# Kernel optimization log

Measured on AMD Instinct MI355X. Metric: run time of the kernel, lower is better.

Reference implementation:

```python
import jax, jax.numpy as jnp
import numpy as np

B, C, H, W = 1, 512, 64, 64
HEADS, DIM_HEAD = 8, 64
GROUPS = 32
EPS = 1e-5
SCALE = DIM_HEAD ** -0.5


def setup_inputs() -> dict:
    key = jax.random.key(0)
    ks = jax.random.split(key, 8)
    inner = HEADS * DIM_HEAD  # 512
    s = 0.02
    return {
        "hidden_states": jax.random.normal(ks[0], (B, C, H, W), jnp.float32),
        "gn_gamma": jnp.ones((C,), jnp.float32),
        "gn_beta": jnp.zeros((C,), jnp.float32),
        "wq": jax.random.normal(ks[1], (inner, C), jnp.float32) * s,
        "wk": jax.random.normal(ks[2], (inner, C), jnp.float32) * s,
        "wv": jax.random.normal(ks[3], (inner, C), jnp.float32) * s,
        "wo": jax.random.normal(ks[4], (C, inner), jnp.float32) * s,
        "bo": jnp.zeros((C,), jnp.float32),
    }


def _group_norm(x, gamma, beta):
    # x: [B, C, H, W]; normalize within channel groups over (C//G, H, W)
    b, c, h, w = x.shape
    xg = x.reshape(b, GROUPS, c // GROUPS, h, w)
    mean = xg.mean(axis=(2, 3, 4), keepdims=True)
    var = xg.var(axis=(2, 3, 4), keepdims=True)
    xg = (xg - mean) * jax.lax.rsqrt(var + EPS)
    x = xg.reshape(b, c, h, w)
    return x * gamma[None, :, None, None] + beta[None, :, None, None]


def reference(hidden_states, gn_gamma, gn_beta, wq, wk, wv, wo, bo):
    residual = hidden_states
    x = _group_norm(hidden_states, gn_gamma, gn_beta)
    b, c, h, w = x.shape
    n = h * w
    x = x.reshape(b, c, n).transpose(0, 2, 1)  # [B, N, C]

    # torch Linear: y = x @ W^T (bias=False for q/k/v)
    q = (x @ wq.T).reshape(b, n, HEADS, DIM_HEAD).transpose(0, 2, 1, 3)  # [B,H,N,D]
    k = (x @ wk.T).reshape(b, n, HEADS, DIM_HEAD).transpose(0, 2, 1, 3)
    v = (x @ wv.T).reshape(b, n, HEADS, DIM_HEAD).transpose(0, 2, 1, 3)

    scores = jnp.einsum("bhqd,bhkd->bhqk", q, k) * SCALE  # [B,H,N,N]
    probs = jax.nn.softmax(scores, axis=-1)
    out = jnp.einsum("bhqk,bhkd->bhqd", probs, v)  # [B,H,N,D]

    out = out.transpose(0, 2, 1, 3).reshape(b, n, HEADS * DIM_HEAD)  # [B,N,inner]
    out = out @ wo.T + bo  # [B,N,C]
    out = out.transpose(0, 2, 1).reshape(b, c, h, w)
    return out + residual
```

## Files before the change

### kernel.cpp

```cpp
#include <hip/hip_runtime.h>

#define N_TOK 4096
#define C_DIM 512
#define NH    8
#define EPS   1e-5f
#define NSPLIT 4
#define THR   11.0f

typedef __attribute__((ext_vector_type(8))) __bf16 bf16x8;
typedef __attribute__((ext_vector_type(4))) float  f32x4;
using u16 = unsigned short;
using u32 = unsigned int;

#define MFMA16 __builtin_amdgcn_mfma_f32_16x16x32_bf16

__device__ __forceinline__ u16 f2bf(float f){
  u32 x = __builtin_bit_cast(u32, f);
  x += 0x7fffu + ((x>>16)&1u);
  return (u16)(x>>16);
}
__device__ __forceinline__ float exp2a(float x){
  float r; asm("v_exp_f32 %0, %1" : "=v"(r) : "v"(x)); return r;
}
__device__ __forceinline__ u32 cvtpk(float lo, float hi){
  u32 r; asm("v_cvt_pk_bf16_f32 %0, %1, %2" : "=v"(r) : "v"(lo), "v"(hi)); return r;
}
__device__ __forceinline__ void dma16(const void* src, void* lds){
  __builtin_amdgcn_global_load_lds(
      (const __attribute__((address_space(1))) u32*)src,
      (__attribute__((address_space(3))) u32*)lds, 16, 0, 0);
}

__global__ __launch_bounds__(256) void k_cvt4(const float* __restrict__ s0,
      const float* __restrict__ s1, const float* __restrict__ s2,
      const float* __restrict__ s3, u16* __restrict__ d0, u16* __restrict__ d1,
      u16* __restrict__ d2, u16* __restrict__ d3){
  int b = blockIdx.x >> 8;
  int i = (blockIdx.x & 255)*256 + threadIdx.x;
  const float* s = b==0?s0 : b==1?s1 : b==2?s2 : s3;
  u16*         d = b==0?d0 : b==1?d1 : b==2?d2 : d3;
  float4 v = ((const float4*)s)[i];
  ushort4 o; o.x=f2bf(v.x); o.y=f2bf(v.y); o.z=f2bf(v.z); o.w=f2bf(v.w);
  ((ushort4*)d)[i] = o;
}

__global__ __launch_bounds__(256) void k_gn_stats(const float* __restrict__ x,
                                                  float* __restrict__ pstat){
  int g = blockIdx.x, p = blockIdx.y, t = threadIdx.x;
  const float4* gx4 = (const float4*)(x + (size_t)g*16*N_TOK) + (size_t)p*2048;
  float s=0.f, ss=0.f;
  #pragma unroll
  for (int k=0;k<8;k++){
    float4 v = gx4[t + k*256];
    s  += v.x+v.y+v.z+v.w;
    ss += v.x*v.x+v.y*v.y+v.z*v.z+v.w*v.w;
  }
  for (int m=1;m<64;m<<=1){ s += __shfl_xor(s,m); ss += __shfl_xor(ss,m); }
  __shared__ float rs[4], rss[4];
  int w=t>>6, lane=t&63;
  if (lane==0){ rs[w]=s; rss[w]=ss; }
  __syncthreads();
  if (t==0){
    pstat[(g*8+p)*2  ] = rs[0]+rs[1]+rs[2]+rs[3];
    pstat[(g*8+p)*2+1] = rss[0]+rss[1]+rss[2]+rss[3];
  }
}

__global__ __launch_bounds__(256) void k_gn_apply(const float* __restrict__ x,
      const float* __restrict__ pstat, const float* __restrict__ gamma,
      const float* __restrict__ beta, u16* __restrict__ X){
  int g = blockIdx.x, c0 = g*16;
  int n = blockIdx.y*256 + threadIdx.x;
  float S=0.f, SS=0.f;
  #pragma unroll
  for (int p=0;p<8;p++){ S += pstat[(g*8+p)*2]; SS += pstat[(g*8+p)*2+1]; }
  float mean = S*(1.f/65536.f);
  float rstd = rsqrtf(SS*(1.f/65536.f) - mean*mean + EPS);
  u16 ov[16];
  #pragma unroll
  for (int c=0;c<16;c++){
    float gm = gamma[c0+c]*rstd;
    float be = beta[c0+c] - mean*gm;
    float v  = x[(size_t)(c0+c)*N_TOK + n]*gm + be;
    ov[c] = f2bf(v);
  }
  uint4* dst = (uint4*)&X[(size_t)n*C_DIM + c0];
  dst[0] = *(uint4*)&ov[0];
  dst[1] = *(uint4*)&ov[8];
}

__device__ __forceinline__ void gemm_core(const u16* A, const u16* B,
      int m0, int n0, char* LDS, f32x4 (&acc)[4][4]){
  int t = threadIdx.x, w = t>>6, l = t&63, lr = l&15, li = l>>4;
  int wr = w>>1, wc = w&1;
  char* As = LDS;
  char* Bs = LDS + 32768;
  const char* Ac = (const char*)A;
  const char* Bc = (const char*)B;
  int ys   = ((l&7)*16) ^ ((l>>3)<<4);
  int rswz = (lr&7)<<4;

  size_t arow[4], brow[4]; int ldst[4];
  #pragma unroll
  for (int r=0;r<4;r++){
    int row = w*32 + r*8 + (l>>3);
    arow[r] = (size_t)(m0+row)*1024 + ys;
    brow[r] = (size_t)(n0+row)*1024 + ys;
    ldst[r] = w*4096 + r*1024;
  }
  #pragma unroll
  for (int r=0;r<4;r++){
    dma16(Ac + arow[r], As + ldst[r]);
    dma16(Bc + brow[r], Bs + ldst[r]);
  }
  __syncthreads();

  int buf = 0;
  for (int it=0; it<8; it++){
    if (it < 7){
      int nb = buf^1;
      #pragma unroll
      for (int r=0;r<4;r++){
        dma16(Ac + arow[r] + (it+1)*128, As + nb*16384 + ldst[r]);
        dma16(Bc + brow[r] + (it+1)*128, Bs + nb*16384 + ldst[r]);
      }
    }
    char* Ab = As + buf*16384;
    char* Bb = Bs + buf*16384;
    #pragma unroll
    for (int ks=0; ks<2; ks++){
      bf16x8 af[4], bfr[4];
      #pragma unroll
      for (int i=0;i<4;i++){
        int rowA = wr*64 + i*16 + lr;
        int rowB = wc*64 + i*16 + lr;
        af[i]  = *(const bf16x8*)(Ab + rowA*128 + ((li*16 + ks*64) ^ rswz));
        bfr[i] = *(const bf16x8*)(Bb + rowB*128 + ((li*16 + ks*64) ^ rswz));
      }
      __builtin_amdgcn_s_setprio(1);
      #pragma unroll
      for (int i=0;i<4;i++){
        #pragma unroll
        for (int j=0;j<4;j++){
          acc[i][j] = MFMA16(af[i], bfr[j], acc[i][j], 0,0,0);
        }
      }
      __builtin_amdgcn_s_setprio(0);
    }
    __syncthreads();
    buf ^= 1;
  }
}

__global__ __launch_bounds__(256,2) void k_qkv2(const u16* __restrict__ X,
      const u16* __restrict__ wq, const u16* __restrict__ wk,
      const u16* __restrict__ wv, u16* __restrict__ Qo, u16* __restrict__ Ko,
      u16* __restrict__ Vto){
  __shared__ char LDS[65536];
  int b = blockIdx.x;
  const u16 *A, *B; u16* Cp; int ldc, m0, n0; float sc = 1.f;
  if (b < 128){        A=X;  B=wq; Cp=Qo;  ldc=512;  m0=(b>>2)*128; n0=(b&3)*128;
                       sc = 0.125f*1.44269504f; }
  else if (b < 256){ int r=b-128; A=X;  B=wk; Cp=Ko;  ldc=512;  m0=(r>>2)*128; n0=(r&3)*128; }
  else             { int r=b-256; A=wv; B=X;  Cp=Vto; ldc=4096; m0=(r>>5)*128; n0=(r&31)*128; }

  f32x4 acc[4][4] = {};
  gemm_core(A, B, m0, n0, LDS, acc);

  int t = threadIdx.x, w = t>>6, l = t&63, lr = l&15, li = l>>4;
  int wr = w>>1, wc = w&1;
  #pragma unroll
  for (int i=0;i<4;i++){
    #pragma unroll
    for (int rr=0;rr<4;rr++){
      int mm = m0 + wr*64 + i*16 + li*4 + rr;
      #pragma unroll
      for (int j=0;j<4;j++){
        int nn = n0 + wc*64 + j*16 + lr;
        Cp[(size_t)mm*ldc + nn] = f2bf(acc[i][j][rr]*sc);
      }
    }
  }
}

__global__ __launch_bounds__(256,2) void k_oproj2(const u16* __restrict__ Wo,
      const u16* __restrict__ Ob, const float* __restrict__ bo,
      const float* __restrict__ res, float* __restrict__ out){
  __shared__ char LDS[65536];
  int r0 = blockIdx.x;
  int m0 = (r0>>5)*128, n0 = (r0&31)*128;

  f32x4 acc[4][4] = {};
  gemm_core(Wo, Ob, m0, n0, LDS, acc);

  int t = threadIdx.x, w = t>>6, l = t&63, lr = l&15, li = l>>4;
  int wr = w>>1, wc = w&1;
  #pragma unroll
  for (int i=0;i<4;i++){
    #pragma unroll
    for (int rr=0;rr<4;rr++){
      int cc = m0 + wr*64 + i*16 + li*4 + rr;
      float bias = bo[cc];
      #pragma unroll
      for (int j=0;j<4;j++){
        int nn = n0 + wc*64 + j*16 + lr;
        size_t off = (size_t)cc*4096 + nn;
        out[off] = acc[i][j][rr] + bias + res[off];
      }
    }
  }
}

__global__ __launch_bounds__(256,4) void k_attn5(const u16* __restrict__ Q,
      const u16* __restrict__ K, const u16* __restrict__ Vt,
      float* __restrict__ Opart, float* __restrict__ ml){
  __shared__ char KV[2][16384];
  int h = blockIdx.y, sp = blockIdx.z;
  int q0 = blockIdx.x*128;
  int t = threadIdx.x, w = t>>6, l = t&63, lr = l&15, li = l>>4;
  char* KVb = (char*)KV;
  int qbase = q0 + w*32;

  const u16* Qp = Q + (size_t)(qbase + lr)*512 + h*64 + li*8;
  bf16x8 qa00 = *(const bf16x8*)(Qp);
  bf16x8 qa01 = *(const bf16x8*)(Qp + 32);
  bf16x8 qa10 = *(const bf16x8*)(Qp + 16*512);
  bf16x8 qa11 = *(const bf16x8*)(Qp + 16*512 + 32);

  int srow = l>>3, y0 = (l&7)*16;
  const char* Kc = (const char*)K;
  const char* Vc = (const char*)Vt;
  const char* ksrc[2]; const char* vsrc[2]; int ldso[2];
  #pragma unroll
  for (int j=0;j<2;j++){
    int row = w*16 + j*8 + srow;
    int ys  = y0 ^ ((row&7)<<4);
    ksrc[j] = Kc + (size_t)(sp*1024 + row)*1024 + h*128 + ys;
    vsrc[j] = Vc + (size_t)(h*64 + row)*8192 + sp*2048 + ys;
    ldso[j] = w*2048 + j*1024;
  }

  #pragma unroll
  for (int j=0;j<2;j++){
    dma16(ksrc[j], KVb + ldso[j]);
    dma16(vsrc[j], KVb + 8192 + ldso[j]);
  }
  __syncthreads();

  f32x4 acc0[4] = {}; f32x4 acc1[4] = {};
  float m0=-1e30f, m1=-1e30f, l0=0.f, l1=0.f;
  int buf = 0;

  for (int it=0; it<16; it++){
    if (it < 15){
      int nb = buf^1;
      #pragma unroll
      for (int j=0;j<2;j++){
        dma16(ksrc[j] + (size_t)(it+1)*65536, KVb + nb*16384 + ldso[j]);
        dma16(vsrc[j] + (it+1)*128,           KVb + nb*16384 + 8192 + ldso[j]);
      }
    }
    char* Klb = KVb + buf*16384;
    char* Vlb = Klb + 8192;

    f32x4 st0[4] = {}; f32x4 st1[4] = {};
    __builtin_amdgcn_s_setprio(1);
    #pragma unroll
    for (int T=0;T<4;T++){
      int row = T*16 + lr, swz = (row&7)<<4;
      const char* rb = Klb + row*128;
      bf16x8 k0 = *(const bf16x8*)(rb + ((li*16     ) ^ swz));
      bf16x8 k1 = *(const bf16x8*)(rb + ((li*16 + 64) ^ swz));
      st0[T] = MFMA16(k0, qa00, st0[T], 0,0,0);
      st0[T] = MFMA16(k1, qa01, st0[T], 0,0,0);
      st1[T] = MFMA16(k0, qa10, st1[T], 0,0,0);
      st1[T] = MFMA16(k1, qa11, st1[T], 0,0,0);
    }
    __builtin_amdgcn_s_setprio(0);

    u32 pk0[8], pk1[8];
    {
      float c0 = fmaxf(fmaxf(st0[0][0],st0[0][1]),fmaxf(st0[0][2],st0[0][3]));
      float c1 = fmaxf(fmaxf(st0[1][0],st0[1][1]),fmaxf(st0[1][2],st0[1][3]));
      float c2 = fmaxf(fmaxf(st0[2][0],st0[2][1]),fmaxf(st0[2][2],st0[2][3]));
      float c3 = fmaxf(fmaxf(st0[3][0],st0[3][1]),fmaxf(st0[3][2],st0[3][3]));
      float pmax = fmaxf(fmaxf(c0,c1),fmaxf(c2,c3));
      pmax = fmaxf(pmax, __shfl_xor(pmax,16));
      pmax = fmaxf(pmax, __shfl_xor(pmax,32));
      if (!__all(pmax <= m0 + THR)){
        float mnew = fmaxf(m0, pmax);
        float fac = exp2a(m0 - mnew);
        m0 = mnew; l0 *= fac;
        float f0=__shfl(fac, li*20+0), f1=__shfl(fac, li*20+1);
        float f2=__shfl(fac, li*20+2), f3=__shfl(fac, li*20+3);
        #pragma unroll
        for (int T=0;T<4;T++){
          acc0[T][0]*=f0; acc0[T][1]*=f1; acc0[T][2]*=f2; acc0[T][3]*=f3;
        }
      }
      float lad = 0.f;
      #pragma unroll
      for (int T=0;T<4;T++){
        float p0=exp2a(st0[T][0]-m0), p1=exp2a(st0[T][1]-m0);
        float p2=exp2a(st0[T][2]-m0), p3=exp2a(st0[T][3]-m0);
        lad += (p0+p1)+(p2+p3);
        pk0[T*2]   = cvtpk(p0,p1);
        pk0[T*2+1] = cvtpk(p2,p3);
      }
      l0 += lad;
    }
    {
      float c0 = fmaxf(fmaxf(st1[0][0],st1[0][1]),fmaxf(st1[0][2],st1[0][3]));
      float c1 = fmaxf(fmaxf(st1[1][0],st1[1][1]),fmaxf(st1[1][2],st1[1][3]));
      float c2 = fmaxf(fmaxf(st1[2][0],st1[2][1]),fmaxf(st1[2][2],st1[2][3]));
      float c3 = fmaxf(fmaxf(st1[3][0],st1[3][1]),fmaxf(st1[3][2],st1[3][3]));
      float pmax = fmaxf(fmaxf(c0,c1),fmaxf(c2,c3));
      pmax = fmaxf(pmax, __shfl_xor(pmax,16));
      pmax = fmaxf(pmax, __shfl_xor(pmax,32));
      if (!__all(pmax <= m1 + THR)){
        float mnew = fmaxf(m1, pmax);
        float fac = exp2a(m1 - mnew);
        m1 = mnew; l1 *= fac;
        float f0=__shfl(fac, li*20+0), f1=__shfl(fac, li*20+1);
        float f2=__shfl(fac, li*20+2), f3=__shfl(fac, li*20+3);
        #pragma unroll
        for (int T=0;T<4;T++){
          acc1[T][0]*=f0; acc1[T][1]*=f1; acc1[T][2]*=f2; acc1[T][3]*=f3;
        }
      }
      float lad = 0.f;
      #pragma unroll
      for (int T=0;T<4;T++){
        float p0=exp2a(st1[T][0]-m1), p1=exp2a(st1[T][1]-m1);
        float p2=exp2a(st1[T][2]-m1), p3=exp2a(st1[T][3]-m1);
        lad += (p0+p1)+(p2+p3);
        pk1[T*2]   = cvtpk(p0,p1);
        pk1[T*2+1] = cvtpk(p2,p3);
      }
      l1 += lad;
    }

    __builtin_amdgcn_s_setprio(1);
    #pragma unroll
    for (int c=0;c<2;c++){
      union { bf16x8 v; u32 u[4]; } A0, A1;
      #pragma unroll
      for (int k=0;k<4;k++){ A0.u[k]=pk0[c*4+k]; A1.u[k]=pk1[c*4+k]; }
      #pragma unroll
      for (int T=0;T<4;T++){
        int vrow = T*16 + lr, vswz = (vrow&7)<<4;
        const char* rb = Vlb + vrow*128;
        union { bf16x8 v; uint2 d[2]; } V2;
        V2.d[0] = *(const uint2*)(rb + ((c*64      + li*8) ^ vswz));
        V2.d[1] = *(const uint2*)(rb + ((c*64 + 32 + li*8) ^ vswz));
        acc0[T] = MFMA16(A0.v, V2.v, acc0[T], 0,0,0);
        acc1[T] = MFMA16(A1.v, V2.v, acc1[T], 0,0,0);
      }
    }
    __builtin_amdgcn_s_setprio(0);

    __syncthreads();
    buf ^= 1;
  }

  l0 += __shfl_xor(l0,16); l0 += __shfl_xor(l0,32);
  l1 += __shfl_xor(l1,16); l1 += __shfl_xor(l1,32);
  float* Op = Opart + (size_t)sp*N_TOK*C_DIM;
  #pragma unroll
  for (int T=0;T<4;T++){
    #pragma unroll
    for (int r=0;r<4;r++){
      Op[(size_t)(qbase      + li*4 + r)*512 + h*64 + T*16 + lr] = acc0[T][r];
      Op[(size_t)(qbase + 16 + li*4 + r)*512 + h*64 + T*16 + lr] = acc1[T][r];
    }
  }
  if (li==0){
    float* p0 = ml + (((size_t)sp*NH + h)*N_TOK + qbase + lr)*2;
    p0[0]=m0; p0[1]=l0;
    float* p1 = ml + (((size_t)sp*NH + h)*N_TOK + qbase + 16 + lr)*2;
    p1[0]=m1; p1[1]=l1;
  }
}

__global__ __launch_bounds__(256) void k_merge(const float* __restrict__ Opart,
      const float* __restrict__ ml, u16* __restrict__ Ob){
  int i  = blockIdx.x*256 + threadIdx.x;
  int q  = i >> 7;
  int c4 = i & 127;
  int h  = c4 >> 4;
  float m[NSPLIT], lv[NSPLIT];
  #pragma unroll
  for (int s=0;s<NSPLIT;s++){
    const float* p = ml + (((size_t)s*NH + h)*N_TOK + q)*2;
    m[s]=p[0]; lv[s]=p[1];
  }
  float M = fmaxf(fmaxf(m[0],m[1]), fmaxf(m[2],m[3]));
  float wgt[NSPLIT]; float L = 0.f;
  #pragma unroll
  for (int s=0;s<NSPLIT;s++){ wgt[s] = exp2a(m[s]-M); L += lv[s]*wgt[s]; }
  float inv = 1.f/L;
  float4 o = {0.f,0.f,0.f,0.f};
  #pragma unroll
  for (int s=0;s<NSPLIT;s++){
    float4 a = ((const float4*)(Opart + (size_t)s*N_TOK*C_DIM))[i];
    o.x += a.x*wgt[s]; o.y += a.y*wgt[s]; o.z += a.z*wgt[s]; o.w += a.w*wgt[s];
  }
  ushort4 r;
  r.x=f2bf(o.x*inv); r.y=f2bf(o.y*inv); r.z=f2bf(o.z*inv); r.w=f2bf(o.w*inv);
  ((ushort4*)Ob)[i] = r;
}

extern "C" void kernel_launch(void* const* d_in, const int* in_sizes, int n_in,
                              void* d_out, int out_size, void* d_ws, size_t ws_size,
                              hipStream_t stream){
  (void)in_sizes; (void)n_in; (void)out_size; (void)ws_size;
  const float* hs    = (const float*)d_in[0];
  const float* gamma = (const float*)d_in[1];
  const float* beta  = (const float*)d_in[2];
  const float* wq    = (const float*)d_in[3];
  const float* wk    = (const float*)d_in[4];
  const float* wv    = (const float*)d_in[5];
  const float* wo    = (const float*)d_in[6];
  const float* bo    = (const float*)d_in[7];
  float* out = (float*)d_out;

  u16* X   = (u16*)d_ws;
  u16* Qb  = X   + (size_t)4096*512;
  u16* Kb  = Qb  + (size_t)4096*512;
  u16* Vtb = Kb  + (size_t)4096*512;
  u16* Ob  = Vtb + (size_t)4096*512;
  u16* wqb = Ob  + (size_t)4096*512;
  u16* wkb = wqb + (size_t)512*512;
  u16* wvb = wkb + (size_t)512*512;
  u16* wob = wvb + (size_t)512*512;
  float* pstat = (float*)(wob + (size_t)512*512);
  float* Opart = pstat + 1024;
  float* mlbuf = Opart + (size_t)NSPLIT*4096*512;

  k_cvt4<<<1024,256,0,stream>>>(wq, wk, wv, wo, wqb, wkb, wvb, wob);
  dim3 gs(32, 8);
  k_gn_stats<<<gs,256,0,stream>>>(hs, pstat);
  dim3 ga(32, 16);
  k_gn_apply<<<ga,256,0,stream>>>(hs, pstat, gamma, beta, X);
  k_qkv2<<<384,256,0,stream>>>(X, wqb, wkb, wvb, Qb, Kb, Vtb);
  dim3 gat(32, 8, NSPLIT);
  k_attn5<<<gat,256,0,stream>>>(Qb, Kb, Vtb, Opart, mlbuf);
  k_merge<<<2048,256,0,stream>>>(Opart, mlbuf, Ob);
  k_oproj2<<<128,256,0,stream>>>(wob, Ob, bo, hs, out);
}
```

Before: 95.79 us.

## Fuse prep kernels, store bf16 attention partials, permute V for single LDS loads

Merges the weight-conversion and group-norm stats kernels into one launch. The split-attention partial outputs are now stored as bf16 instead of fp32, halving the write and read traffic between attention and merge. V^T is written with a token permutation so each attention lane fetches its V fragment with one 16-byte LDS read instead of two 8-byte reads. Max reductions use v_max3. The bf16 partials lower the precision of the intermediate results.

```diff
diff --git a/kernel.cpp b/kernel.cpp
--- a/kernel.cpp
+++ b/kernel.cpp
@@ -19,11 +19,17 @@
   x += 0x7fffu + ((x>>16)&1u);
   return (u16)(x>>16);
 }
+__device__ __forceinline__ float bf2f(u16 v){
+  return __builtin_bit_cast(float, (u32)v<<16);
+}
 __device__ __forceinline__ float exp2a(float x){
   float r; asm("v_exp_f32 %0, %1" : "=v"(r) : "v"(x)); return r;
 }
 __device__ __forceinline__ u32 cvtpk(float lo, float hi){
   u32 r; asm("v_cvt_pk_bf16_f32 %0, %1, %2" : "=v"(r) : "v"(lo), "v"(hi)); return r;
+}
+__device__ __forceinline__ float max3a(float a, float b, float c){
+  float r; asm("v_max3_f32 %0, %1, %2, %3" : "=v"(r) : "v"(a), "v"(b), "v"(c)); return r;
 }
 __device__ __forceinline__ void dma16(const void* src, void* lds){
   __builtin_amdgcn_global_load_lds(
@@ -31,22 +37,25 @@
       (__attribute__((address_space(3))) u32*)lds, 16, 0, 0);
 }
 
-__global__ __launch_bounds__(256) void k_cvt4(const float* __restrict__ s0,
+__global__ __launch_bounds__(256) void k_pre(const float* __restrict__ s0,
       const float* __restrict__ s1, const float* __restrict__ s2,
       const float* __restrict__ s3, u16* __restrict__ d0, u16* __restrict__ d1,
-      u16* __restrict__ d2, u16* __restrict__ d3){
-  int b = blockIdx.x >> 8;
-  int i = (blockIdx.x & 255)*256 + threadIdx.x;
-  const float* s = b==0?s0 : b==1?s1 : b==2?s2 : s3;
-  u16*         d = b==0?d0 : b==1?d1 : b==2?d2 : d3;
-  float4 v = ((const float4*)s)[i];
-  ushort4 o; o.x=f2bf(v.x); o.y=f2bf(v.y); o.z=f2bf(v.z); o.w=f2bf(v.w);
-  ((ushort4*)d)[i] = o;
-}
-
-__global__ __launch_bounds__(256) void k_gn_stats(const float* __restrict__ x,
-                                                  float* __restrict__ pstat){
-  int g = blockIdx.x, p = blockIdx.y, t = threadIdx.x;
+      u16* __restrict__ d2, u16* __restrict__ d3,
+      const float* __restrict__ x, float* __restrict__ pstat){
+  __shared__ float rs[4], rss[4];
+  int b = blockIdx.x;
+  if (b < 1024){
+    int m = b >> 8;
+    int i = (b & 255)*256 + threadIdx.x;
+    const float* s = m==0?s0 : m==1?s1 : m==2?s2 : s3;
+    u16*         d = m==0?d0 : m==1?d1 : m==2?d2 : d3;
+    float4 v = ((const float4*)s)[i];
+    ushort4 o; o.x=f2bf(v.x); o.y=f2bf(v.y); o.z=f2bf(v.z); o.w=f2bf(v.w);
+    ((ushort4*)d)[i] = o;
+    return;
+  }
+  int gb = b - 1024;
+  int g = gb>>3, p = gb&7, t = threadIdx.x;
   const float4* gx4 = (const float4*)(x + (size_t)g*16*N_TOK) + (size_t)p*2048;
   float s=0.f, ss=0.f;
   #pragma unroll
@@ -56,7 +65,6 @@
     ss += v.x*v.x+v.y*v.y+v.z*v.z+v.w*v.w;
   }
   for (int m=1;m<64;m<<=1){ s += __shfl_xor(s,m); ss += __shfl_xor(ss,m); }
-  __shared__ float rs[4], rss[4];
   int w=t>>6, lane=t&63;
   if (lane==0){ rs[w]=s; rss[w]=ss; }
   __syncthreads();
@@ -158,11 +166,12 @@
       u16* __restrict__ Vto){
   __shared__ char LDS[65536];
   int b = blockIdx.x;
-  const u16 *A, *B; u16* Cp; int ldc, m0, n0; float sc = 1.f;
+  const u16 *A, *B; u16* Cp; int ldc, m0, n0; float sc = 1.f; bool vperm = false;
   if (b < 128){        A=X;  B=wq; Cp=Qo;  ldc=512;  m0=(b>>2)*128; n0=(b&3)*128;
                        sc = 0.125f*1.44269504f; }
   else if (b < 256){ int r=b-128; A=X;  B=wk; Cp=Ko;  ldc=512;  m0=(r>>2)*128; n0=(r&3)*128; }
-  else             { int r=b-256; A=wv; B=X;  Cp=Vto; ldc=4096; m0=(r>>5)*128; n0=(r&31)*128; }
+  else             { int r=b-256; A=wv; B=X;  Cp=Vto; ldc=4096; m0=(r>>5)*128; n0=(r&31)*128;
+                     vperm = true; }
 
   f32x4 acc[4][4] = {};
   gemm_core(A, B, m0, n0, LDS, acc);
@@ -177,6 +186,11 @@
       #pragma unroll
       for (int j=0;j<4;j++){
         int nn = n0 + wc*64 + j*16 + lr;
+        if (vperm){
+          int tl = nn & 63;
+          int pos = (tl & 35) | ((tl & 12) << 1) | ((tl & 16) >> 2);
+          nn = (nn & ~63) | pos;
+        }
         Cp[(size_t)mm*ldc + nn] = f2bf(acc[i][j][rr]*sc);
       }
     }
@@ -211,9 +225,9 @@
   }
 }
 
-__global__ __launch_bounds__(256,4) void k_attn5(const u16* __restrict__ Q,
+__global__ __launch_bounds__(256,4) void k_attn6(const u16* __restrict__ Q,
       const u16* __restrict__ K, const u16* __restrict__ Vt,
-      float* __restrict__ Opart, float* __restrict__ ml){
+      u16* __restrict__ Opart, float* __restrict__ ml){
   __shared__ char KV[2][16384];
   int h = blockIdx.y, sp = blockIdx.z;
   int q0 = blockIdx.x*128;
@@ -280,11 +294,12 @@
 
     u32 pk0[8], pk1[8];
     {
-      float c0 = fmaxf(fmaxf(st0[0][0],st0[0][1]),fmaxf(st0[0][2],st0[0][3]));
-      float c1 = fmaxf(fmaxf(st0[1][0],st0[1][1]),fmaxf(st0[1][2],st0[1][3]));
-      float c2 = fmaxf(fmaxf(st0[2][0],st0[2][1]),fmaxf(st0[2][2],st0[2][3]));
-      float c3 = fmaxf(fmaxf(st0[3][0],st0[3][1]),fmaxf(st0[3][2],st0[3][3]));
-      float pmax = fmaxf(fmaxf(c0,c1),fmaxf(c2,c3));
+      float a0 = max3a(st0[0][0],st0[0][1],st0[0][2]);
+      float a1 = max3a(st0[1][0],st0[1][1],st0[1][2]);
+      float a2 = max3a(st0[2][0],st0[2][1],st0[2][2]);
+      float a3 = max3a(st0[3][0],st0[3][1],st0[3][2]);
+      float b0 = max3a(st0[0][3],st0[1][3],st0[2][3]);
+      float pmax = fmaxf(max3a(a0,a1,a2), max3a(a3,b0,st0[3][3]));
       pmax = fmaxf(pmax, __shfl_xor(pmax,16));
       pmax = fmaxf(pmax, __shfl_xor(pmax,32));
       if (!__all(pmax <= m0 + THR)){
@@ -310,11 +325,12 @@
       l0 += lad;
     }
     {
-      float c0 = fmaxf(fmaxf(st1[0][0],st1[0][1]),fmaxf(st1[0][2],st1[0][3]));
-      float c1 = fmaxf(fmaxf(st1[1][0],st1[1][1]),fmaxf(st1[1][2],st1[1][3]));
-      float c2 = fmaxf(fmaxf(st1[2][0],st1[2][1]),fmaxf(st1[2][2],st1[2][3]));
-      float c3 = fmaxf(fmaxf(st1[3][0],st1[3][1]),fmaxf(st1[3][2],st1[3][3]));
-      float pmax = fmaxf(fmaxf(c0,c1),fmaxf(c2,c3));
+      float a0 = max3a(st1[0][0],st1[0][1],st1[0][2]);
+      float a1 = max3a(st1[1][0],st1[1][1],st1[1][2]);
+      float a2 = max3a(st1[2][0],st1[2][1],st1[2][2]);
+      float a3 = max3a(st1[3][0],st1[3][1],st1[3][2]);
+      float b0 = max3a(st1[0][3],st1[1][3],st1[2][3]);
+      float pmax = fmaxf(max3a(a0,a1,a2), max3a(a3,b0,st1[3][3]));
       pmax = fmaxf(pmax, __shfl_xor(pmax,16));
       pmax = fmaxf(pmax, __shfl_xor(pmax,32));
       if (!__all(pmax <= m1 + THR)){
@@ -349,12 +365,9 @@
       #pragma unroll
       for (int T=0;T<4;T++){
         int vrow = T*16 + lr, vswz = (vrow&7)<<4;
-        const char* rb = Vlb + vrow*128;
-        union { bf16x8 v; uint2 d[2]; } V2;
-        V2.d[0] = *(const uint2*)(rb + ((c*64      + li*8) ^ vswz));
-        V2.d[1] = *(const uint2*)(rb + ((c*64 + 32 + li*8) ^ vswz));
-        acc0[T] = MFMA16(A0.v, V2.v, acc0[T], 0,0,0);
-        acc1[T] = MFMA16(A1.v, V2.v, acc1[T], 0,0,0);
+        bf16x8 vb = *(const bf16x8*)(Vlb + vrow*128 + ((c*64 + li*16) ^ vswz));
+        acc0[T] = MFMA16(A0.v, vb, acc0[T], 0,0,0);
+        acc1[T] = MFMA16(A1.v, vb, acc1[T], 0,0,0);
       }
     }
     __builtin_amdgcn_s_setprio(0);
@@ -365,13 +378,13 @@
 
   l0 += __shfl_xor(l0,16); l0 += __shfl_xor(l0,32);
   l1 += __shfl_xor(l1,16); l1 += __shfl_xor(l1,32);
-  float* Op = Opart + (size_t)sp*N_TOK*C_DIM;
+  u16* Op = Opart + (size_t)sp*N_TOK*C_DIM;
   #pragma unroll
   for (int T=0;T<4;T++){
     #pragma unroll
     for (int r=0;r<4;r++){
-      Op[(size_t)(qbase      + li*4 + r)*512 + h*64 + T*16 + lr] = acc0[T][r];
-      Op[(size_t)(qbase + 16 + li*4 + r)*512 + h*64 + T*16 + lr] = acc1[T][r];
+      Op[(size_t)(qbase      + li*4 + r)*512 + h*64 + T*16 + lr] = f2bf(acc0[T][r]);
+      Op[(size_t)(qbase + 16 + li*4 + r)*512 + h*64 + T*16 + lr] = f2bf(acc1[T][r]);
     }
   }
   if (li==0){
@@ -382,7 +395,7 @@
   }
 }
 
-__global__ __launch_bounds__(256) void k_merge(const float* __restrict__ Opart,
+__global__ __launch_bounds__(256) void k_merge2(const u16* __restrict__ Opart,
       const float* __restrict__ ml, u16* __restrict__ Ob){
   int i  = blockIdx.x*256 + threadIdx.x;
   int q  = i >> 7;
@@ -394,7 +407,7 @@
     const float* p = ml + (((size_t)s*NH + h)*N_TOK + q)*2;
     m[s]=p[0]; lv[s]=p[1];
   }
-  float M = fmaxf(fmaxf(m[0],m[1]), fmaxf(m[2],m[3]));
+  float M = fmaxf(max3a(m[0],m[1],m[2]), m[3]);
   float wgt[NSPLIT]; float L = 0.f;
   #pragma unroll
   for (int s=0;s<NSPLIT;s++){ wgt[s] = exp2a(m[s]-M); L += lv[s]*wgt[s]; }
@@ -402,8 +415,9 @@
   float4 o = {0.f,0.f,0.f,0.f};
   #pragma unroll
   for (int s=0;s<NSPLIT;s++){
-    float4 a = ((const float4*)(Opart + (size_t)s*N_TOK*C_DIM))[i];
-    o.x += a.x*wgt[s]; o.y += a.y*wgt[s]; o.z += a.z*wgt[s]; o.w += a.w*wgt[s];
+    ushort4 a = ((const ushort4*)(Opart + (size_t)s*N_TOK*C_DIM))[i];
+    o.x += bf2f(a.x)*wgt[s]; o.y += bf2f(a.y)*wgt[s];
+    o.z += bf2f(a.z)*wgt[s]; o.w += bf2f(a.w)*wgt[s];
   }
   ushort4 r;
   r.x=f2bf(o.x*inv); r.y=f2bf(o.y*inv); r.z=f2bf(o.z*inv); r.w=f2bf(o.w*inv);
@@ -434,17 +448,15 @@
   u16* wvb = wkb + (size_t)512*512;
   u16* wob = wvb + (size_t)512*512;
   float* pstat = (float*)(wob + (size_t)512*512);
-  float* Opart = pstat + 1024;
-  float* mlbuf = Opart + (size_t)NSPLIT*4096*512;
-
-  k_cvt4<<<1024,256,0,stream>>>(wq, wk, wv, wo, wqb, wkb, wvb, wob);
-  dim3 gs(32, 8);
-  k_gn_stats<<<gs,256,0,stream>>>(hs, pstat);
+  u16* Opart   = (u16*)(pstat + 1024);
+  float* mlbuf = (float*)(Opart + (size_t)NSPLIT*4096*512);
+
+  k_pre<<<1280,256,0,stream>>>(wq, wk, wv, wo, wqb, wkb, wvb, wob, hs, pstat);
   dim3 ga(32, 16);
   k_gn_apply<<<ga,256,0,stream>>>(hs, pstat, gamma, beta, X);
   k_qkv2<<<384,256,0,stream>>>(X, wqb, wkb, wvb, Qb, Kb, Vtb);
   dim3 gat(32, 8, NSPLIT);
-  k_attn5<<<gat,256,0,stream>>>(Qb, Kb, Vtb, Opart, mlbuf);
-  k_merge<<<2048,256,0,stream>>>(Opart, mlbuf, Ob);
+  k_attn6<<<gat,256,0,stream>>>(Qb, Kb, Vtb, Opart, mlbuf);
+  k_merge2<<<2048,256,0,stream>>>(Opart, mlbuf, Ob);
   k_oproj2<<<128,256,0,stream>>>(wob, Ob, bo, hs, out);
 }
```

Result: faster. 85.99 us (-10.2%).
